# Optimization experiments

Measured on AMD Instinct MI355X. Metric: run time of the kernel, lower is better.

Reference implementation:

```python
import jax, jax.numpy as jnp
import numpy as np

N = 100000
E = 1600000
D_IN = 128
D_H = 128


def _sage_conv(x, src, dst, W_self, W_neigh, b, n_nodes):
    # mean aggregation over in-neighbors: dst receives from src
    gathered = x[src]                                        # [E, D]
    summed = jax.ops.segment_sum(gathered, dst, num_segments=n_nodes)  # [N, D]
    deg = jax.ops.segment_sum(jnp.ones((src.shape[0],), x.dtype), dst,
                              num_segments=n_nodes)          # [N]
    mean_neigh = summed / jnp.maximum(deg, 1.0)[:, None]     # zero-degree -> 0
    return x @ W_self + mean_neigh @ W_neigh + b


def setup_inputs() -> dict:
    key = jax.random.key(0)
    ks = jax.random.split(key, 9)
    s1 = 1.0 / np.sqrt(D_IN)
    s2 = 1.0 / np.sqrt(D_H)
    return {
        "in_feat": jax.random.normal(ks[0], (N, D_IN), jnp.float32),
        "W1_self": jax.random.uniform(ks[1], (D_IN, D_H), jnp.float32, -s1, s1),
        "W1_neigh": jax.random.uniform(ks[2], (D_IN, D_H), jnp.float32, -s1, s1),
        "b1": jnp.zeros((D_H,), jnp.float32),
        "W2_self": jax.random.uniform(ks[3], (D_H, D_H), jnp.float32, -s2, s2),
        "W2_neigh": jax.random.uniform(ks[4], (D_H, D_H), jnp.float32, -s2, s2),
        "b2": jnp.zeros((D_H,), jnp.float32),
        "src": jax.random.randint(ks[5], (E,), 0, N, jnp.int32),
        "dst": jax.random.randint(ks[6], (E,), 0, N, jnp.int32),
    }


def reference(in_feat, W1_self, W1_neigh, b1, W2_self, W2_neigh, b2, src, dst):
    h = _sage_conv(in_feat, src, dst, W1_self, W1_neigh, b1, N)
    h = jax.nn.relu(h)
    h = _sage_conv(h, src, dst, W2_self, W2_neigh, b2, N)
    return h
```

## Files before the change

kernel.cpp:

```cpp
#include <hip/hip_runtime.h>
#include <hip/hip_fp16.h>

#define D 128
#define NB_MAX 1024
#define PART_BLOCKS 512

using f32x4  = __attribute__((ext_vector_type(4))) float;
using half8  = __attribute__((ext_vector_type(8))) _Float16;
using short8 = __attribute__((ext_vector_type(8))) short;

#define AS1(p) ((const __attribute__((address_space(1))) void*)(p))
#define AS3(p) ((__attribute__((address_space(3))) void*)(p))

__global__ void prep_k(const float* __restrict__ x, __half* __restrict__ y, int n4,
                       const float* __restrict__ W1s, const float* __restrict__ W1n,
                       const float* __restrict__ W2s, const float* __restrict__ W2n,
                       unsigned short* __restrict__ Wg1, unsigned short* __restrict__ Wg2,
                       int* __restrict__ bucket_counts, int nb, int xb) {
    int b = blockIdx.x;
    int t = threadIdx.x;
    if (b < xb) {
        int i = b * 256 + t;
        if (i < n4) {
            float4 v = *(const float4*)(x + (size_t)i * 4);
            __half2 h0 = __floats2half2_rn(v.x, v.y);
            __half2 h1 = __floats2half2_rn(v.z, v.w);
            __half2* o = (__half2*)(y + (size_t)i * 4);
            o[0] = h0; o[1] = h1;
        }
        return;
    }
    int wb = b - xb;
    if (wb < 512) {
        int sel = wb >> 8;
        int lb  = wb & 255;
        if (lb >= 128) return;
        const float* Ws = sel ? W2s : W1s;
        const float* Wn = sel ? W2n : W1n;
        unsigned short* Wg = sel ? Wg2 : Wg1;
        int idx = lb * 256 + t;
        int col = idx >> 8;
        int k   = idx & 255;
        float v = (k < 128) ? Ws[k * D + col] : Wn[(k - 128) * D + col];
        _Float16 hv = (_Float16)v;
        _Float16 lv = (_Float16)(v - (float)hv);
        int kc = k >> 5, q = (k >> 3) & 3, j = k & 7;
        Wg[(((kc * 2 + 0) * 4 + q) * 128 + col) * 8 + j] = *(unsigned short*)&hv;
        Wg[(((kc * 2 + 1) * 4 + q) * 128 + col) * 8 + j] = *(unsigned short*)&lv;
        return;
    }
    int i = (wb - 512) * 256 + t;
    if (i < nb) bucket_counts[i] = 0;
}

__global__ void bucket_count_k(const int* __restrict__ dst, int* __restrict__ bucket_counts,
                               int E, int nb) {
    __shared__ int hist[NB_MAX];
    int t = threadIdx.x;
    for (int b = t; b < nb; b += 256) hist[b] = 0;
    __syncthreads();
    for (int i = blockIdx.x * 256 + t; i < E; i += gridDim.x * 256)
        atomicAdd(&hist[dst[i] >> 8], 1);
    __syncthreads();
    for (int b = t; b < nb; b += 256) {
        int c = hist[b];
        if (c) atomicAdd(&bucket_counts[b], c);
    }
}

__global__ void bucket_scan_k(const int* __restrict__ bucket_counts,
                              int* __restrict__ bucket_base,
                              int* __restrict__ bucket_cursor, int nb) {
    __shared__ int sh[256];
    int t = threadIdx.x;
    int base = t * 4;
    int v0 = (base + 0 < nb) ? bucket_counts[base + 0] : 0;
    int v1 = (base + 1 < nb) ? bucket_counts[base + 1] : 0;
    int v2 = (base + 2 < nb) ? bucket_counts[base + 2] : 0;
    int v3 = (base + 3 < nb) ? bucket_counts[base + 3] : 0;
    int tsum = v0 + v1 + v2 + v3;
    sh[t] = tsum;
    __syncthreads();
    for (int off = 1; off < 256; off <<= 1) {
        int x = 0;
        if (t >= off) x = sh[t - off];
        __syncthreads();
        if (t >= off) sh[t] += x;
        __syncthreads();
    }
    int excl = sh[t] - tsum;
    if (base + 0 < nb) { bucket_base[base+0] = excl;          bucket_cursor[base+0] = excl; }
    if (base + 1 < nb) { bucket_base[base+1] = excl+v0;       bucket_cursor[base+1] = excl+v0; }
    if (base + 2 < nb) { bucket_base[base+2] = excl+v0+v1;    bucket_cursor[base+2] = excl+v0+v1; }
    if (base + 3 < nb) { bucket_base[base+3] = excl+v0+v1+v2; bucket_cursor[base+3] = excl+v0+v1+v2; }
    if (t == 255) bucket_base[nb] = sh[255];
}

__global__ void partition_k(const int* __restrict__ src, const int* __restrict__ dst,
                            int* __restrict__ bucket_cursor, unsigned* __restrict__ pairs,
                            int E, int nb, int chunk) {
    __shared__ int hist[NB_MAX];
    __shared__ int bbase[NB_MAX];
    int t = threadIdx.x;
    int e0 = blockIdx.x * chunk;
    int e1 = min(E, e0 + chunk);
    for (int b = t; b < nb; b += 256) hist[b] = 0;
    __syncthreads();
    for (int i = e0 + t; i < e1; i += 256)
        atomicAdd(&hist[dst[i] >> 8], 1);
    __syncthreads();
    for (int b = t; b < nb; b += 256) {
        int c = hist[b];
        int bs = 0;
        if (c) bs = atomicAdd(&bucket_cursor[b], c);
        bbase[b] = bs;
        hist[b] = 0;
    }
    __syncthreads();
    for (int i = e0 + t; i < e1; i += 256) {
        int dd = dst[i];
        int b = dd >> 8;
        int r = atomicAdd(&hist[b], 1);
        pairs[bbase[b] + r] = ((unsigned)(dd & 255) << 17) | (unsigned)src[i];
    }
}

__global__ void build_csr_k(const unsigned* __restrict__ pairs,
                            const int* __restrict__ bucket_base,
                            int* __restrict__ counts, int* __restrict__ offsets,
                            int* __restrict__ edge_src, int N) {
    __shared__ int hist[256];
    __shared__ int curs[256];
    __shared__ int sh[256];
    int t = threadIdx.x;
    int b = blockIdx.x;
    int n0 = b << 8;
    int e0 = bucket_base[b];
    int e1 = bucket_base[b + 1];
    hist[t] = 0;
    __syncthreads();
    for (int i = e0 + t; i < e1; i += 256)
        atomicAdd(&hist[pairs[i] >> 17], 1);
    __syncthreads();
    int c = hist[t];
    sh[t] = c;
    __syncthreads();
    for (int off = 1; off < 256; off <<= 1) {
        int x = 0;
        if (t >= off) x = sh[t - off];
        __syncthreads();
        if (t >= off) sh[t] += x;
        __syncthreads();
    }
    int excl = sh[t] - c;
    curs[t] = excl;
    int node = n0 + t;
    if (node < N) { counts[node] = c; offsets[node] = e0 + excl; }
    __syncthreads();
    for (int i = e0 + t; i < e1; i += 256) {
        unsigned p = pairs[i];
        int pos = atomicAdd(&curs[p >> 17], 1);
        edge_src[e0 + pos] = (int)(p & 0x1FFFFu);
    }
}

__global__ void aggregate_f16_k(const __half* __restrict__ x,
                                const int* __restrict__ edge_src,
                                const int* __restrict__ offsets,
                                const int* __restrict__ counts,
                                __half* __restrict__ agg, int n) {
    int wid  = (blockIdx.x * blockDim.x + threadIdx.x) >> 6;
    int lane = threadIdx.x & 63;
    if (wid >= n) return;
    int sg  = lane >> 4;
    int sub = lane & 15;
    int start = offsets[wid];
    int cnt   = counts[wid];
    float acc[8] = {0.f, 0.f, 0.f, 0.f, 0.f, 0.f, 0.f, 0.f};
    for (int base = 0; base < cnt; base += 64) {
        int valid = min(64, cnt - base);
        int s = (lane < valid) ? edge_src[start + base + lane] : 0;
        for (int k0 = 0; k0 < valid; k0 += 16) {
            float4 raw[4];
            float  wg[4];
            #pragma unroll
            for (int u = 0; u < 4; ++u) {
                int idx = k0 + 4 * u + sg;
                int row = __shfl(s, idx & 63);
                wg[u] = (idx < valid) ? 1.0f : 0.0f;
                raw[u] = *(const float4*)(x + (size_t)row * D + sub * 8);
            }
            #pragma unroll
            for (int u = 0; u < 4; ++u) {
                const __half2* hp = (const __half2*)&raw[u];
                #pragma unroll
                for (int j = 0; j < 4; ++j) {
                    float2 f = __half22float2(hp[j]);
                    acc[2 * j]     = fmaf(f.x, wg[u], acc[2 * j]);
                    acc[2 * j + 1] = fmaf(f.y, wg[u], acc[2 * j + 1]);
                }
            }
        }
    }
    #pragma unroll
    for (int j = 0; j < 8; ++j) {
        acc[j] += __shfl(acc[j], lane ^ 16);
        acc[j] += __shfl(acc[j], lane ^ 32);
    }
    if (sg == 0) {
        float inv = 1.0f / fmaxf((float)cnt, 1.0f);
        union { __half2 h2[4]; short8 s8; } u;
        #pragma unroll
        for (int j = 0; j < 4; ++j)
            u.h2[j] = __floats2half2_rn(acc[2 * j] * inv, acc[2 * j + 1] * inv);
        *(short8*)(agg + (size_t)wid * D + sub * 8) = u.s8;
    }
}

__global__ __launch_bounds__(512)
void mfma_gemm_k(const _Float16* __restrict__ A0, const _Float16* __restrict__ A1,
                 const unsigned short* __restrict__ Wg,
                 const float* __restrict__ bias,
                 float* __restrict__ C, __half* __restrict__ Ch,
                 int n, int out_mode) {
    __shared__ __align__(16) unsigned short lds_b[8192];
    int t = threadIdx.x;
    int w = t >> 6;
    int l = t & 63;
    int m = l & 15;
    int q = l >> 4;
    int r0 = blockIdx.x * 256 + w * 32;

    f32x4 acc[2][8];
    #pragma unroll
    for (int rt = 0; rt < 2; ++rt)
        #pragma unroll
        for (int ct = 0; ct < 8; ++ct)
            acc[rt][ct] = (f32x4){0.f, 0.f, 0.f, 0.f};

    for (int kc = 0; kc < 8; ++kc) {
        const unsigned short* gk = Wg + (size_t)kc * 8192;
        #pragma unroll
        for (int i = 0; i < 2; ++i) {
            int e = i * 512 + t;
            __builtin_amdgcn_global_load_lds(AS1(gk + e * 8), AS3(lds_b + e * 8), 16, 0, 0);
        }
        const _Float16* __restrict__ A = (kc < 4) ? A0 : A1;
        int ka = (kc & 3) * 32;
        half8 a[2];
        #pragma unroll
        for (int rt = 0; rt < 2; ++rt) {
            int row = r0 + rt * 16 + m;
            half8 v = (half8){0, 0, 0, 0, 0, 0, 0, 0};
            if (row < n) v = *(const half8*)(A + (size_t)row * D + ka + q * 8);
            a[rt] = v;
        }
        __syncthreads();

        #pragma unroll
        for (int ct = 0; ct < 8; ++ct) {
            half8 bh = *(const half8*)&lds_b[(size_t)(q * 128 + ct * 16 + m) * 8];
            half8 bl = *(const half8*)&lds_b[(size_t)((4 + q) * 128 + ct * 16 + m) * 8];
            #pragma unroll
            for (int rt = 0; rt < 2; ++rt) {
                acc[rt][ct] = __builtin_amdgcn_mfma_f32_16x16x32_f16(a[rt], bh, acc[rt][ct], 0, 0, 0);
                acc[rt][ct] = __builtin_amdgcn_mfma_f32_16x16x32_f16(a[rt], bl, acc[rt][ct], 0, 0, 0);
            }
        }
        __syncthreads();
    }

    #pragma unroll
    for (int ct = 0; ct < 8; ++ct) {
        int col = ct * 16 + m;
        float bb = bias[col];
        #pragma unroll
        for (int rt = 0; rt < 2; ++rt) {
            #pragma unroll
            for (int r = 0; r < 4; ++r) {
                int row = r0 + rt * 16 + q * 4 + r;
                if (row < n) {
                    float v = acc[rt][ct][r] + bb;
                    if (out_mode) {
                        v = fmaxf(v, 0.f);
                        Ch[(size_t)row * D + col] = __float2half(v);
                    } else {
                        C[(size_t)row * D + col] = v;
                    }
                }
            }
        }
    }
}

extern "C" void kernel_launch(void* const* d_in, const int* in_sizes, int n_in,
                              void* d_out, int out_size, void* d_ws, size_t ws_size,
                              hipStream_t stream) {
    const float* in_feat = (const float*)d_in[0];
    const float* W1s     = (const float*)d_in[1];
    const float* W1n     = (const float*)d_in[2];
    const float* b1      = (const float*)d_in[3];
    const float* W2s     = (const float*)d_in[4];
    const float* W2n     = (const float*)d_in[5];
    const float* b2      = (const float*)d_in[6];
    const int*   src     = (const int*)d_in[7];
    const int*   dst     = (const int*)d_in[8];

    const int N  = in_sizes[0] / D;
    const int E  = in_sizes[7];
    const int NB = (N + 255) >> 8;

    char* base = (char*)d_ws;
    size_t off = 0;
    __half* agg16 = (__half*)(base + off); off += (size_t)N * D * 2;
    __half* xh16  = (__half*)(base + off); off += (size_t)N * D * 2;
    int* edge_src = (int*)(base + off);    off += (size_t)E * 4;
    int* counts   = (int*)(base + off);    off += (size_t)N * 4;
    int* offsets  = (int*)(base + off);    off += (size_t)N * 4;
    unsigned short* Wg1 = (unsigned short*)(base + off); off += 65536 * 2;
    unsigned short* Wg2 = (unsigned short*)(base + off); off += 65536 * 2;
    int* bucket_counts = (int*)(base + off); off += NB_MAX * 4;
    int* bucket_base   = (int*)(base + off); off += (NB_MAX + 1) * 4;
    off = (off + 15) & ~(size_t)15;
    int* bucket_cursor = (int*)(base + off); off += NB_MAX * 4;

    unsigned* pairs = (unsigned*)agg16;

    const int chunk = (E + PART_BLOCKS - 1) / PART_BLOCKS;
    const int n4 = (N * D) / 4;
    const int xb = (n4 + 255) / 256;
    const int zb = (NB + 255) / 256;

    hipLaunchKernelGGL(prep_k, dim3(xb + 512 + zb), dim3(256), 0, stream,
                       in_feat, xh16, n4, W1s, W1n, W2s, W2n, Wg1, Wg2,
                       bucket_counts, NB, xb);

    hipLaunchKernelGGL(bucket_count_k, dim3(PART_BLOCKS), dim3(256), 0, stream,
                       dst, bucket_counts, E, NB);
    hipLaunchKernelGGL(bucket_scan_k, dim3(1), dim3(256), 0, stream,
                       bucket_counts, bucket_base, bucket_cursor, NB);
    hipLaunchKernelGGL(partition_k, dim3(PART_BLOCKS), dim3(256), 0, stream,
                       src, dst, bucket_cursor, pairs, E, NB, chunk);
    hipLaunchKernelGGL(build_csr_k, dim3(NB), dim3(256), 0, stream,
                       pairs, bucket_base, counts, offsets, edge_src, N);

    const dim3 aggGrid(((size_t)N * 64 + 255) / 256);
    const dim3 gemmGrid((N + 255) / 256);

    hipLaunchKernelGGL(aggregate_f16_k, aggGrid, dim3(256), 0, stream,
                       xh16, edge_src, offsets, counts, agg16, N);
    hipLaunchKernelGGL(mfma_gemm_k, gemmGrid, dim3(512), 0, stream,
                       (const _Float16*)xh16, (const _Float16*)agg16, Wg1, b1,
                       (float*)nullptr, xh16, N, 1);

    hipLaunchKernelGGL(aggregate_f16_k, aggGrid, dim3(256), 0, stream,
                       xh16, edge_src, offsets, counts, agg16, N);
    hipLaunchKernelGGL(mfma_gemm_k, gemmGrid, dim3(512), 0, stream,
                       (const _Float16*)xh16, (const _Float16*)agg16, Wg2, b2,
                       (float*)d_out, (__half*)nullptr, N, 0);
}
```

Measured before the change: 352.4 us.

## Pack four nodes per wave in aggregation and double-buffer GEMM weight tiles

The aggregation kernel now gives each 16-lane group of a wave its own destination node instead of spreading one node across all 64 lanes. This removes the cross-lane reduction and the idle lanes that occur when a node has few edges (average degree is about 16), but each wave now loops to the largest degree among its four nodes. The GEMM moves to 256-thread blocks of 128 rows and double-buffers the weight chunk in LDS and the A fragments in registers, so the next chunk loads while MFMAs run, at the cost of twice the LDS per block. The partition block count is also halved.

```diff
diff --git a/kernel.cpp b/kernel.cpp
--- a/kernel.cpp
+++ b/kernel.cpp
@@ -3,7 +3,7 @@
 
 #define D 128
 #define NB_MAX 1024
-#define PART_BLOCKS 512
+#define PART_BLOCKS 256
 
 using f32x4  = __attribute__((ext_vector_type(4))) float;
 using half8  = __attribute__((ext_vector_type(8))) _Float16;
@@ -168,68 +168,65 @@
                                 const int* __restrict__ edge_src,
                                 const int* __restrict__ offsets,
                                 const int* __restrict__ counts,
-                                __half* __restrict__ agg, int n) {
-    int wid  = (blockIdx.x * blockDim.x + threadIdx.x) >> 6;
-    int lane = threadIdx.x & 63;
-    if (wid >= n) return;
-    int sg  = lane >> 4;
-    int sub = lane & 15;
-    int start = offsets[wid];
-    int cnt   = counts[wid];
+                                __half* __restrict__ agg, int n, int E1) {
+    int gwave = (blockIdx.x * blockDim.x + threadIdx.x) >> 6;
+    int lane  = threadIdx.x & 63;
+    int slot  = lane >> 4;
+    int sub   = lane & 15;
+    int node  = gwave * 4 + slot;
+    bool act  = node < n;
+    int start = act ? offsets[node] : 0;
+    int cnt   = act ? counts[node] : 0;
+    int mc = cnt;
+    mc = max(mc, __shfl(mc, lane ^ 16));
+    mc = max(mc, __shfl(mc, lane ^ 32));
     float acc[8] = {0.f, 0.f, 0.f, 0.f, 0.f, 0.f, 0.f, 0.f};
-    for (int base = 0; base < cnt; base += 64) {
-        int valid = min(64, cnt - base);
-        int s = (lane < valid) ? edge_src[start + base + lane] : 0;
-        for (int k0 = 0; k0 < valid; k0 += 16) {
-            float4 raw[4];
-            float  wg[4];
-            #pragma unroll
-            for (int u = 0; u < 4; ++u) {
-                int idx = k0 + 4 * u + sg;
-                int row = __shfl(s, idx & 63);
-                wg[u] = (idx < valid) ? 1.0f : 0.0f;
-                raw[u] = *(const float4*)(x + (size_t)row * D + sub * 8);
-            }
-            #pragma unroll
-            for (int u = 0; u < 4; ++u) {
-                const __half2* hp = (const __half2*)&raw[u];
+    for (int base = 0; base < mc; base += 16) {
+        int ids = edge_src[min(start + base + sub, E1)];
+        #pragma unroll
+        for (int h = 0; h < 2; ++h) {
+            float4 raw[8];
+            float  wg[8];
+            #pragma unroll
+            for (int r = 0; r < 8; ++r) {
+                int e = base + h * 8 + r;
+                int row = __shfl(ids, (lane & 48) | (h * 8 + r));
+                wg[r] = (e < cnt) ? 1.0f : 0.0f;
+                raw[r] = *(const float4*)(x + (size_t)row * D + sub * 8);
+            }
+            #pragma unroll
+            for (int r = 0; r < 8; ++r) {
+                union { float4 f4; half8 h8; } cv;
+                cv.f4 = raw[r];
                 #pragma unroll
-                for (int j = 0; j < 4; ++j) {
-                    float2 f = __half22float2(hp[j]);
-                    acc[2 * j]     = fmaf(f.x, wg[u], acc[2 * j]);
-                    acc[2 * j + 1] = fmaf(f.y, wg[u], acc[2 * j + 1]);
-                }
-            }
-        }
-    }
-    #pragma unroll
-    for (int j = 0; j < 8; ++j) {
-        acc[j] += __shfl(acc[j], lane ^ 16);
-        acc[j] += __shfl(acc[j], lane ^ 32);
-    }
-    if (sg == 0) {
+                for (int j = 0; j < 8; ++j)
+                    acc[j] = fmaf((float)cv.h8[j], wg[r], acc[j]);
+            }
+        }
+    }
+    if (act) {
         float inv = 1.0f / fmaxf((float)cnt, 1.0f);
         union { __half2 h2[4]; short8 s8; } u;
         #pragma unroll
         for (int j = 0; j < 4; ++j)
             u.h2[j] = __floats2half2_rn(acc[2 * j] * inv, acc[2 * j + 1] * inv);
-        *(short8*)(agg + (size_t)wid * D + sub * 8) = u.s8;
-    }
-}
-
-__global__ __launch_bounds__(512)
+        *(short8*)(agg + (size_t)node * D + sub * 8) = u.s8;
+    }
+}
+
+__global__ __launch_bounds__(256)
 void mfma_gemm_k(const _Float16* __restrict__ A0, const _Float16* __restrict__ A1,
                  const unsigned short* __restrict__ Wg,
                  const float* __restrict__ bias,
                  float* __restrict__ C, __half* __restrict__ Ch,
                  int n, int out_mode) {
-    __shared__ __align__(16) unsigned short lds_b[8192];
+    __shared__ __align__(16) unsigned short lds_b[2][8192];
     int t = threadIdx.x;
     int w = t >> 6;
     int l = t & 63;
     int m = l & 15;
     int q = l >> 4;
-    int r0 = blockIdx.x * 256 + w * 32;
+    int r0 = blockIdx.x * 128 + w * 32;
 
     f32x4 acc[2][8];
     #pragma unroll
@@ -238,36 +235,53 @@
         for (int ct = 0; ct < 8; ++ct)
             acc[rt][ct] = (f32x4){0.f, 0.f, 0.f, 0.f};
 
+    #pragma unroll
+    for (int i = 0; i < 4; ++i) {
+        int e = i * 256 + t;
+        __builtin_amdgcn_global_load_lds(AS1(Wg + e * 8), AS3(&lds_b[0][e * 8]), 16, 0, 0);
+    }
+    half8 a_cur[2], a_nxt[2];
+    a_nxt[0] = a_nxt[1] = (half8){0, 0, 0, 0, 0, 0, 0, 0};
+    #pragma unroll
+    for (int rt = 0; rt < 2; ++rt) {
+        int row = r0 + rt * 16 + m;
+        half8 v = (half8){0, 0, 0, 0, 0, 0, 0, 0};
+        if (row < n) v = *(const half8*)(A0 + (size_t)row * D + q * 8);
+        a_cur[rt] = v;
+    }
+
     for (int kc = 0; kc < 8; ++kc) {
-        const unsigned short* gk = Wg + (size_t)kc * 8192;
-        #pragma unroll
-        for (int i = 0; i < 2; ++i) {
-            int e = i * 512 + t;
-            __builtin_amdgcn_global_load_lds(AS1(gk + e * 8), AS3(lds_b + e * 8), 16, 0, 0);
-        }
-        const _Float16* __restrict__ A = (kc < 4) ? A0 : A1;
-        int ka = (kc & 3) * 32;
-        half8 a[2];
-        #pragma unroll
-        for (int rt = 0; rt < 2; ++rt) {
-            int row = r0 + rt * 16 + m;
-            half8 v = (half8){0, 0, 0, 0, 0, 0, 0, 0};
-            if (row < n) v = *(const half8*)(A + (size_t)row * D + ka + q * 8);
-            a[rt] = v;
-        }
-        __syncthreads();
-
+        int p = kc & 1;
+        __syncthreads();
+        if (kc < 7) {
+            const unsigned short* gk = Wg + (size_t)(kc + 1) * 8192;
+            #pragma unroll
+            for (int i = 0; i < 4; ++i) {
+                int e = i * 256 + t;
+                __builtin_amdgcn_global_load_lds(AS1(gk + e * 8), AS3(&lds_b[1 - p][e * 8]), 16, 0, 0);
+            }
+            const _Float16* __restrict__ An = ((kc + 1) < 4) ? A0 : A1;
+            int kan = ((kc + 1) & 3) * 32;
+            #pragma unroll
+            for (int rt = 0; rt < 2; ++rt) {
+                int row = r0 + rt * 16 + m;
+                half8 v = (half8){0, 0, 0, 0, 0, 0, 0, 0};
+                if (row < n) v = *(const half8*)(An + (size_t)row * D + kan + q * 8);
+                a_nxt[rt] = v;
+            }
+        }
         #pragma unroll
         for (int ct = 0; ct < 8; ++ct) {
-            half8 bh = *(const half8*)&lds_b[(size_t)(q * 128 + ct * 16 + m) * 8];
-            half8 bl = *(const half8*)&lds_b[(size_t)((4 + q) * 128 + ct * 16 + m) * 8];
+            half8 bh = *(const half8*)&lds_b[p][(size_t)(q * 128 + ct * 16 + m) * 8];
+            half8 bl = *(const half8*)&lds_b[p][(size_t)((4 + q) * 128 + ct * 16 + m) * 8];
             #pragma unroll
             for (int rt = 0; rt < 2; ++rt) {
-                acc[rt][ct] = __builtin_amdgcn_mfma_f32_16x16x32_f16(a[rt], bh, acc[rt][ct], 0, 0, 0);
-                acc[rt][ct] = __builtin_amdgcn_mfma_f32_16x16x32_f16(a[rt], bl, acc[rt][ct], 0, 0, 0);
-            }
-        }
-        __syncthreads();
+                acc[rt][ct] = __builtin_amdgcn_mfma_f32_16x16x32_f16(a_cur[rt], bh, acc[rt][ct], 0, 0, 0);
+                acc[rt][ct] = __builtin_amdgcn_mfma_f32_16x16x32_f16(a_cur[rt], bl, acc[rt][ct], 0, 0, 0);
+            }
+        }
+        a_cur[0] = a_nxt[0];
+        a_cur[1] = a_nxt[1];
     }
 
     #pragma unroll
@@ -344,18 +358,19 @@
     hipLaunchKernelGGL(build_csr_k, dim3(NB), dim3(256), 0, stream,
                        pairs, bucket_base, counts, offsets, edge_src, N);
 
-    const dim3 aggGrid(((size_t)N * 64 + 255) / 256);
-    const dim3 gemmGrid((N + 255) / 256);
+    const int nwaves = (N + 3) / 4;
+    const dim3 aggGrid(((size_t)nwaves * 64 + 255) / 256);
+    const dim3 gemmGrid((N + 127) / 128);
 
     hipLaunchKernelGGL(aggregate_f16_k, aggGrid, dim3(256), 0, stream,
-                       xh16, edge_src, offsets, counts, agg16, N);
-    hipLaunchKernelGGL(mfma_gemm_k, gemmGrid, dim3(512), 0, stream,
+                       xh16, edge_src, offsets, counts, agg16, N, E - 1);
+    hipLaunchKernelGGL(mfma_gemm_k, gemmGrid, dim3(256), 0, stream,
                        (const _Float16*)xh16, (const _Float16*)agg16, Wg1, b1,
                        (float*)nullptr, xh16, N, 1);
 
     hipLaunchKernelGGL(aggregate_f16_k, aggGrid, dim3(256), 0, stream,
-                       xh16, edge_src, offsets, counts, agg16, N);
-    hipLaunchKernelGGL(mfma_gemm_k, gemmGrid, dim3(512), 0, stream,
+                       xh16, edge_src, offsets, counts, agg16, N, E - 1);
+    hipLaunchKernelGGL(mfma_gemm_k, gemmGrid, dim3(256), 0, stream,
                        (const _Float16*)xh16, (const _Float16*)agg16, Wg2, b2,
                        (float*)d_out, (__half*)nullptr, N, 0);
 }
```

After: 434.4 us. +23.3%, slower.

## Aggregate four nodes per wavefront with 16-lane groups instead of one node per wave

Applied to the files above, without the earlier changes.

The mean aggregation kernel now gives each 16-lane group of a wavefront its own destination node, so one wave handles four nodes at once. The cross-group shuffle reduction goes away, and edge indices are loaded 16 at a time per group. Each lane issues eight row loads per half-iteration to keep more memory requests in flight. The cost is divergence from degree imbalance: all four groups loop to the maximum degree among them, with masked zero-weight loads of row 0.

```diff
diff --git a/kernel.cpp b/kernel.cpp
--- a/kernel.cpp
+++ b/kernel.cpp
@@ -169,51 +169,49 @@
                                 const int* __restrict__ offsets,
                                 const int* __restrict__ counts,
                                 __half* __restrict__ agg, int n) {
-    int wid  = (blockIdx.x * blockDim.x + threadIdx.x) >> 6;
-    int lane = threadIdx.x & 63;
-    if (wid >= n) return;
-    int sg  = lane >> 4;
-    int sub = lane & 15;
-    int start = offsets[wid];
-    int cnt   = counts[wid];
+    int gwave = (blockIdx.x * blockDim.x + threadIdx.x) >> 6;
+    int lane  = threadIdx.x & 63;
+    int slot  = lane >> 4;
+    int sub   = lane & 15;
+    int node  = gwave * 4 + slot;
+    bool act  = node < n;
+    int start = act ? offsets[node] : 0;
+    int cnt   = act ? counts[node] : 0;
+    int mc = cnt;
+    mc = max(mc, __shfl(mc, lane ^ 16));
+    mc = max(mc, __shfl(mc, lane ^ 32));
     float acc[8] = {0.f, 0.f, 0.f, 0.f, 0.f, 0.f, 0.f, 0.f};
-    for (int base = 0; base < cnt; base += 64) {
-        int valid = min(64, cnt - base);
-        int s = (lane < valid) ? edge_src[start + base + lane] : 0;
-        for (int k0 = 0; k0 < valid; k0 += 16) {
-            float4 raw[4];
-            float  wg[4];
+    for (int base = 0; base < mc; base += 16) {
+        int e   = base + sub;
+        int ids = (e < cnt) ? edge_src[start + e] : 0;
+        #pragma unroll
+        for (int h = 0; h < 2; ++h) {
+            float4 raw[8];
+            float  wg[8];
             #pragma unroll
-            for (int u = 0; u < 4; ++u) {
-                int idx = k0 + 4 * u + sg;
-                int row = __shfl(s, idx & 63);
-                wg[u] = (idx < valid) ? 1.0f : 0.0f;
-                raw[u] = *(const float4*)(x + (size_t)row * D + sub * 8);
+            for (int r = 0; r < 8; ++r) {
+                int ei  = base + h * 8 + r;
+                int row = __shfl(ids, (lane & 48) | (h * 8 + r));
+                wg[r]  = (ei < cnt) ? 1.0f : 0.0f;
+                raw[r] = *(const float4*)(x + (size_t)row * D + sub * 8);
             }
             #pragma unroll
-            for (int u = 0; u < 4; ++u) {
-                const __half2* hp = (const __half2*)&raw[u];
+            for (int r = 0; r < 8; ++r) {
+                union { float4 f4; half8 h8; } cv;
+                cv.f4 = raw[r];
                 #pragma unroll
-                for (int j = 0; j < 4; ++j) {
-                    float2 f = __half22float2(hp[j]);
-                    acc[2 * j]     = fmaf(f.x, wg[u], acc[2 * j]);
-                    acc[2 * j + 1] = fmaf(f.y, wg[u], acc[2 * j + 1]);
-                }
+                for (int j = 0; j < 8; ++j)
+                    acc[j] = fmaf((float)cv.h8[j], wg[r], acc[j]);
             }
         }
     }
-    #pragma unroll
-    for (int j = 0; j < 8; ++j) {
-        acc[j] += __shfl(acc[j], lane ^ 16);
-        acc[j] += __shfl(acc[j], lane ^ 32);
-    }
-    if (sg == 0) {
+    if (act) {
         float inv = 1.0f / fmaxf((float)cnt, 1.0f);
         union { __half2 h2[4]; short8 s8; } u;
         #pragma unroll
         for (int j = 0; j < 4; ++j)
             u.h2[j] = __floats2half2_rn(acc[2 * j] * inv, acc[2 * j + 1] * inv);
-        *(short8*)(agg + (size_t)wid * D + sub * 8) = u.s8;
+        *(short8*)(agg + (size_t)node * D + sub * 8) = u.s8;
     }
 }
 
@@ -344,7 +342,8 @@
     hipLaunchKernelGGL(build_csr_k, dim3(NB), dim3(256), 0, stream,
                        pairs, bucket_base, counts, offsets, edge_src, N);
 
-    const dim3 aggGrid(((size_t)N * 64 + 255) / 256);
+    const int nwaves = (N + 3) / 4;
+    const dim3 aggGrid(((size_t)nwaves * 64 + 255) / 256);
     const dim3 gemmGrid((N + 255) / 256);
 
     hipLaunchKernelGGL(aggregate_f16_k, aggGrid, dim3(256), 0, stream,
```

New measurement: 355.1 us. About the same (+0.7%).
